# Optimization experiments

Measured on AMD Instinct MI355X. Metric: run time of the kernel, lower is better.

Reference implementation:

```python
import jax, jax.numpy as jnp
import numpy as np
import math

B, N_NODES, N_EDGES = 2, 20000, 320000
IN_DIM, MODEL_DIM, NUM_HEADS = 128, 128, 8
HEAD_DIM = MODEL_DIM // NUM_HEADS
EPS = 1e-5


def setup_inputs() -> dict:
    key = jax.random.key(0)
    ks = jax.random.split(key, 12)
    s = 0.02
    x = jax.random.normal(ks[0], (B, N_NODES, IN_DIM), dtype=jnp.float32)
    edge_index = jax.random.randint(ks[1], (2, N_EDGES), 0, N_NODES, dtype=jnp.int32)
    return {
        "x": x,
        "proj_w": jax.random.normal(ks[2], (IN_DIM, MODEL_DIM), jnp.float32) * s,
        "wq_w": jax.random.normal(ks[3], (MODEL_DIM, MODEL_DIM), jnp.float32) * s,
        "wq_b": jax.random.normal(ks[4], (MODEL_DIM,), jnp.float32) * s,
        "wk_w": jax.random.normal(ks[5], (MODEL_DIM, MODEL_DIM), jnp.float32) * s,
        "wk_b": jax.random.normal(ks[6], (MODEL_DIM,), jnp.float32) * s,
        "wv_w": jax.random.normal(ks[7], (MODEL_DIM, MODEL_DIM), jnp.float32) * s,
        "wv_b": jax.random.normal(ks[8], (MODEL_DIM,), jnp.float32) * s,
        "ln_g": jnp.ones((MODEL_DIM,), jnp.float32),
        "ln_b": jnp.zeros((MODEL_DIM,), jnp.float32),
        "edge_index": edge_index,
    }


def reference(x, proj_w, wq_w, wq_b, wk_w, wk_b, wv_w, wv_b, ln_g, ln_b, edge_index):
    src, dst = edge_index[0], edge_index[1]
    scale = 1.0 / math.sqrt(HEAD_DIM)

    h = x @ proj_w                      # [B, N, D]  (dropout = identity in eval)
    lifted = h[:, src, :]               # [B, E, D] edge gather
    Q = lifted @ wq_w + wq_b
    K = lifted @ wk_w + wk_b
    V = lifted @ wv_w + wv_b

    alpha = jnp.sum(Q * K, axis=-1) * scale  # [B, E]

    def seg_softmax(a):  # a: [E]
        m = jax.ops.segment_max(a, dst, num_segments=N_NODES)
        m = jnp.where(jnp.isfinite(m), m, 0.0)
        e = jnp.exp(a - m[dst])
        s = jax.ops.segment_sum(e, dst, num_segments=N_NODES)
        return e / s[dst]

    attn = jax.vmap(seg_softmax)(alpha)           # [B, E]
    weighted_V = V * attn[..., None]              # [B, E, D]

    seg_sum = lambda t: jax.ops.segment_sum(t, dst, num_segments=N_NODES)
    agg = jax.vmap(seg_sum)(weighted_V)           # [B, N, D]

    counts = jax.ops.segment_sum(jnp.ones((N_EDGES,), jnp.float32), dst,
                                 num_segments=N_NODES)
    skip = jax.vmap(seg_sum)(lifted) / jnp.maximum(counts, 1.0)[None, :, None]

    out = agg + skip
    mu = jnp.mean(out, axis=-1, keepdims=True)
    var = jnp.var(out, axis=-1, keepdims=True)
    return (out - mu) * jax.lax.rsqrt(var + EPS) * ln_g + ln_b
```

## Files before the change

### kernel.cpp

```cpp
#include <hip/hip_runtime.h>
#include <hip/hip_bf16.h>

#define NNODES 20000
#define NEDGES 320000
#define BATCH  2
#define D      128
#define EPSF   1e-5f
#define QTILE_M 64
#define XS_LD   136
#define MAXDEG 64

typedef __attribute__((ext_vector_type(8))) short bf16x8;
typedef __attribute__((ext_vector_type(4))) float f32x4;

static __device__ __forceinline__ unsigned short f2bf(float f) {
    __hip_bfloat16 h = __float2bfloat16(f);
    return *reinterpret_cast<unsigned short*>(&h);
}
static __device__ __forceinline__ float bfu(unsigned short u) {
    union { unsigned int i; float f; } cv;
    cv.i = ((unsigned int)u) << 16;
    return cv.f;
}

__global__ __launch_bounds__(256) void prep_kernel(
    const float* __restrict__ Wp, const float* __restrict__ Wq,
    const float* __restrict__ Wk, const float* __restrict__ Wv,
    unsigned short* __restrict__ WF)
{
    int sg = blockIdx.x * 256 + threadIdx.x;
    int mat = sg >> 11, rem = sg & 2047;
    int f = rem >> 6, l = rem & 63;
    int nt = f >> 2, ks = f & 3;
    int c = l & 15, g = l >> 4;
    const float* W = (mat == 0) ? Wp : (mat == 1) ? Wq : (mat == 2) ? Wk : Wv;
    int n = nt * 16 + c;
    #pragma unroll
    for (int i = 0; i < 8; ++i) {
        int k = ks * 32 + g * 8 + i;
        WF[(size_t)sg * 8 + i] = f2bf(W[k * 128 + n]);
    }
}

__global__ __launch_bounds__(256) void scatter_pad_kernel(
    const int* __restrict__ src, const int* __restrict__ dst,
    const float* __restrict__ a,
    int* __restrict__ cursor,
    int* __restrict__ srcs_pad,
    float* __restrict__ aval)
{
    int e = blockIdx.x * 256 + threadIdx.x;
    if (e >= NEDGES) return;
    int d = dst[e], s = src[e];
    int slot = atomicAdd(&cursor[d], 1);
    if (slot < MAXDEG) {
        int p = d * MAXDEG + slot;
        srcs_pad[p] = s;
        aval[p] = a[s];
        aval[NNODES * MAXDEG + p] = a[NNODES + s];
    }
}

__global__ __launch_bounds__(256) void qkv_mfma_kernel(
    const float* __restrict__ x,
    const unsigned short* __restrict__ WF,
    const float* __restrict__ Bq, const float* __restrict__ Bk, const float* __restrict__ Bv,
    unsigned short* __restrict__ h_out,
    unsigned short* __restrict__ hv_out,
    float* __restrict__ a_out)
{
    __shared__ unsigned short Wbuf[16384];
    __shared__ unsigned short Hs[QTILE_M][XS_LD];
    const int t = threadIdx.x;
    const long row0 = (long)blockIdx.x * QTILE_M;
    const int w = t >> 6, l = t & 63;
    const int g = l >> 4, c = l & 15;
    const int rw = w * 16;

    #define STAGE_W(MAT_OFF)                                            \
        _Pragma("unroll")                                               \
        for (int q = 0; q < 8; ++q) {                                   \
            int s = q * 256 + t;                                        \
            *(bf16x8*)&Wbuf[s * 8] = *(const bf16x8*)(WF + (MAT_OFF) + s * 8); \
        }

    bf16x8 ax[4];
    {
        const float* xr = x + (row0 + rw + c) * D;
        #pragma unroll
        for (int ks = 0; ks < 4; ++ks) {
            float4 u0 = *(const float4*)(xr + ks * 32 + g * 8);
            float4 u1 = *(const float4*)(xr + ks * 32 + g * 8 + 4);
            bf16x8 f;
            f[0] = (short)f2bf(u0.x); f[1] = (short)f2bf(u0.y);
            f[2] = (short)f2bf(u0.z); f[3] = (short)f2bf(u0.w);
            f[4] = (short)f2bf(u1.x); f[5] = (short)f2bf(u1.y);
            f[6] = (short)f2bf(u1.z); f[7] = (short)f2bf(u1.w);
            ax[ks] = f;
        }
    }

    STAGE_W(0)
    __syncthreads();

    f32x4 hacc[8];
    #pragma unroll
    for (int nt = 0; nt < 8; ++nt) hacc[nt] = f32x4{0.f, 0.f, 0.f, 0.f};
    #pragma unroll
    for (int nt = 0; nt < 8; ++nt)
        #pragma unroll
        for (int ks = 0; ks < 4; ++ks) {
            bf16x8 b = *(const bf16x8*)&Wbuf[((nt * 4 + ks) * 64 + l) * 8];
            hacc[nt] = __builtin_amdgcn_mfma_f32_16x16x32_bf16(ax[ks], b, hacc[nt], 0, 0, 0);
        }
    #pragma unroll
    for (int nt = 0; nt < 8; ++nt)
        #pragma unroll
        for (int i = 0; i < 4; ++i)
            Hs[rw + 4 * g + i][nt * 16 + c] = f2bf(hacc[nt][i]);
    __syncthreads();

    #pragma unroll
    for (int q = 0; q < 4; ++q) {
        int ch = t + q * 256;
        int r = ch >> 4, off = (ch & 15) << 3;
        *(bf16x8*)(h_out + (row0 + r) * D + off) = *(const bf16x8*)&Hs[r][off];
    }
    bf16x8 ah[4];
    #pragma unroll
    for (int ks = 0; ks < 4; ++ks)
        ah[ks] = *(const bf16x8*)&Hs[rw + c][ks * 32 + g * 8];
    STAGE_W(16384)
    __syncthreads();

    f32x4 qacc[8];
    #pragma unroll
    for (int nt = 0; nt < 8; ++nt) qacc[nt] = f32x4{0.f, 0.f, 0.f, 0.f};
    #pragma unroll
    for (int nt = 0; nt < 8; ++nt)
        #pragma unroll
        for (int ks = 0; ks < 4; ++ks) {
            bf16x8 b = *(const bf16x8*)&Wbuf[((nt * 4 + ks) * 64 + l) * 8];
            qacc[nt] = __builtin_amdgcn_mfma_f32_16x16x32_bf16(ah[ks], b, qacc[nt], 0, 0, 0);
        }
    __syncthreads();
    STAGE_W(32768)
    __syncthreads();

    f32x4 kacc[8];
    #pragma unroll
    for (int nt = 0; nt < 8; ++nt) kacc[nt] = f32x4{0.f, 0.f, 0.f, 0.f};
    #pragma unroll
    for (int nt = 0; nt < 8; ++nt)
        #pragma unroll
        for (int ks = 0; ks < 4; ++ks) {
            bf16x8 b = *(const bf16x8*)&Wbuf[((nt * 4 + ks) * 64 + l) * 8];
            kacc[nt] = __builtin_amdgcn_mfma_f32_16x16x32_bf16(ah[ks], b, kacc[nt], 0, 0, 0);
        }
    __syncthreads();
    STAGE_W(49152)

    {
        float p[4] = {0.f, 0.f, 0.f, 0.f};
        #pragma unroll
        for (int nt = 0; nt < 8; ++nt) {
            float bq = Bq[nt * 16 + c];
            float bk = Bk[nt * 16 + c];
            #pragma unroll
            for (int i = 0; i < 4; ++i)
                p[i] += (qacc[nt][i] + bq) * (kacc[nt][i] + bk);
        }
        #pragma unroll
        for (int off = 1; off < 16; off <<= 1)
            #pragma unroll
            for (int i = 0; i < 4; ++i) p[i] += __shfl_xor(p[i], off, 64);
        if (c == 0)
            #pragma unroll
            for (int i = 0; i < 4; ++i)
                a_out[row0 + rw + 4 * g + i] = p[i] * 0.25f;
    }
    __syncthreads();

    f32x4 vacc[8];
    #pragma unroll
    for (int nt = 0; nt < 8; ++nt) vacc[nt] = f32x4{0.f, 0.f, 0.f, 0.f};
    #pragma unroll
    for (int nt = 0; nt < 8; ++nt)
        #pragma unroll
        for (int ks = 0; ks < 4; ++ks) {
            bf16x8 b = *(const bf16x8*)&Wbuf[((nt * 4 + ks) * 64 + l) * 8];
            vacc[nt] = __builtin_amdgcn_mfma_f32_16x16x32_bf16(ah[ks], b, vacc[nt], 0, 0, 0);
        }
    #pragma unroll
    for (int nt = 0; nt < 8; ++nt) {
        float bv = Bv[nt * 16 + c];
        #pragma unroll
        for (int i = 0; i < 4; ++i)
            Hs[rw + 4 * g + i][nt * 16 + c] = f2bf(vacc[nt][i] + bv);
    }
    __syncthreads();
    #pragma unroll
    for (int q = 0; q < 4; ++q) {
        int ch = t + q * 256;
        int r = ch >> 4, off = (ch & 15) << 3;
        *(bf16x8*)(hv_out + (row0 + r) * D + off) = *(const bf16x8*)&Hs[r][off];
    }
    #undef STAGE_W
}


__global__ __launch_bounds__(256) void agg_kernel(
    const unsigned short* __restrict__ hb,
    const unsigned short* __restrict__ hvb,
    const float* __restrict__ aval,
    const int* __restrict__ deg_arr,
    const int* __restrict__ srcs_pad,
    const float* __restrict__ ln_g, const float* __restrict__ ln_b,
    float* __restrict__ out)
{
    const int t = threadIdx.x;
    const int w = t >> 6, l = t & 63;
    const int flat = blockIdx.x * 4 + w;
    const int n = flat % NNODES;
    const int b = flat / NNODES;
    const int bN = b * NNODES;
    const int deg = min(deg_arr[n], MAXDEG);
    const int base = n * MAXDEG;
    const bool valid = l < deg;

    int   sr_l = valid ? srcs_pad[base + l] : 0;
    float av_l = valid ? aval[b * (NNODES * MAXDEG) + base + l] : -1e30f;

    float m = av_l;
    #pragma unroll
    for (int off = 32; off >= 1; off >>= 1) m = fmaxf(m, __shfl_xor(m, off, 64));
    float e_l = valid ? __expf(av_l - m) : 0.f;
    float s = e_l;
    #pragma unroll
    for (int off = 32; off >= 1; off >>= 1) s += __shfl_xor(s, off, 64);
    const float inv_s = (deg > 0) ? 1.f / s : 0.f;
    const float inv_d = 1.f / (float)max(deg, 1);
    const float w_l = e_l * inv_s;

    const int q4 = l >> 4;
    const int cq = l & 15;
    float acc[8] = {0,0,0,0,0,0,0,0};
    float sk [8] = {0,0,0,0,0,0,0,0};
    const long rowArr = (long)bN * D;

    const int iters = (deg + 3) >> 2;
    for (int jj = 0; jj < iters; ++jj) {
        int sel = (jj << 2) + q4;
        bool ev = sel < deg;
        int selc = ev ? sel : 0;
        int srj  = __shfl(sr_l, selc, 64);
        float wj = __shfl(w_l,  selc, 64);
        wj = ev ? wj : 0.f;
        float skw = ev ? 1.f : 0.f;
        long ofs = rowArr + (long)srj * D + (cq << 3);
        bf16x8 hv8 = *(const bf16x8*)(hvb + ofs);
        bf16x8 h8  = *(const bf16x8*)(hb + ofs);
        #pragma unroll
        for (int i = 0; i < 8; ++i) {
            acc[i] += wj  * bfu((unsigned short)hv8[i]);
            sk[i]  += skw * bfu((unsigned short)h8[i]);
        }
    }

    #pragma unroll
    for (int i = 0; i < 8; ++i) {
        acc[i] += __shfl_xor(acc[i], 32, 64);
        sk[i]  += __shfl_xor(sk[i],  32, 64);
        acc[i] += __shfl_xor(acc[i], 16, 64);
        sk[i]  += __shfl_xor(sk[i],  16, 64);
    }
    float v[8];
    float sum = 0.f, sq = 0.f;
    #pragma unroll
    for (int i = 0; i < 8; ++i) {
        v[i] = acc[i] + sk[i] * inv_d;
        sum += v[i];
        sq  += v[i] * v[i];
    }
    #pragma unroll
    for (int off = 8; off >= 1; off >>= 1) {
        sum += __shfl_xor(sum, off, 64);
        sq  += __shfl_xor(sq,  off, 64);
    }
    float mu   = sum * (1.f / 128.f);
    float var  = sq * (1.f / 128.f) - mu * mu;
    float rstd = rsqrtf(var + EPSF);
    if (q4 == 0) {
        float4 g0 = *(const float4*)(ln_g + (cq << 3));
        float4 g1 = *(const float4*)(ln_g + (cq << 3) + 4);
        float4 b0 = *(const float4*)(ln_b + (cq << 3));
        float4 b1 = *(const float4*)(ln_b + (cq << 3) + 4);
        float4 o0, o1;
        o0.x = (v[0] - mu) * rstd * g0.x + b0.x;
        o0.y = (v[1] - mu) * rstd * g0.y + b0.y;
        o0.z = (v[2] - mu) * rstd * g0.z + b0.z;
        o0.w = (v[3] - mu) * rstd * g0.w + b0.w;
        o1.x = (v[4] - mu) * rstd * g1.x + b1.x;
        o1.y = (v[5] - mu) * rstd * g1.y + b1.y;
        o1.z = (v[6] - mu) * rstd * g1.z + b1.z;
        o1.w = (v[7] - mu) * rstd * g1.w + b1.w;
        float* op = out + (long)flat * D + (cq << 3);
        *(float4*)op = o0;
        *(float4*)(op + 4) = o1;
    }
}


extern "C" void kernel_launch(void* const* d_in, const int* in_sizes, int n_in,
                              void* d_out, int out_size, void* d_ws, size_t ws_size,
                              hipStream_t stream)
{
    const float* x    = (const float*)d_in[0];
    const float* Wp   = (const float*)d_in[1];
    const float* Wq   = (const float*)d_in[2];
    const float* Bq   = (const float*)d_in[3];
    const float* Wk   = (const float*)d_in[4];
    const float* Bk   = (const float*)d_in[5];
    const float* Wv   = (const float*)d_in[6];
    const float* Bv   = (const float*)d_in[7];
    const float* ln_g = (const float*)d_in[8];
    const float* ln_b = (const float*)d_in[9];
    const int*   ei   = (const int*)d_in[10];
    const int* esrc = ei;
    const int* edst = ei + NEDGES;
    float* out = (float*)d_out;

    char* p = (char*)d_ws;
    auto alloc = [&](size_t bytes) -> char* {
        char* r = p;
        p += (bytes + 255) & ~(size_t)255;
        return r;
    };
    unsigned short* hb  = (unsigned short*)alloc((size_t)BATCH * NNODES * D * 2);
    unsigned short* hvb = (unsigned short*)alloc((size_t)BATCH * NNODES * D * 2);
    float* a        = (float*)alloc((size_t)BATCH * NNODES * 4);
    int* cursor     = (int*)alloc((size_t)NNODES * 4);
    int* srcs_pad   = (int*)alloc((size_t)NNODES * MAXDEG * 4);
    float* aval     = (float*)alloc((size_t)BATCH * NNODES * MAXDEG * 4);
    unsigned short* WF = (unsigned short*)alloc((size_t)4 * 128 * 128 * 2);

    hipMemsetAsync(cursor, 0, (size_t)NNODES * 4, stream);
    prep_kernel<<<32, 256, 0, stream>>>(Wp, Wq, Wk, Wv, WF);
    qkv_mfma_kernel<<<(BATCH * NNODES) / QTILE_M, 256, 0, stream>>>(
        x, WF, Bq, Bk, Bv, hb, hvb, a);
    scatter_pad_kernel<<<(NEDGES + 255) / 256, 256, 0, stream>>>(
        esrc, edst, a, cursor, srcs_pad, aval);
    agg_kernel<<<(BATCH * NNODES) / 4, 256, 0, stream>>>(
        hb, hvb, aval, cursor, srcs_pad, ln_g, ln_b, out);
}
```

Baseline: 177.6 us.

## Interleave h/hv rows, drop aval buffer, fuse cursor clear, prefetch weights and gathers

Stores h and hv interleaved in one 256-wide row so each gathered source node reads one contiguous 512-byte span. The scatter kernel no longer writes the per-edge aval array; agg_kernel instead looks up the attention score a[src] itself. The cursor memset is folded into prep_kernel and scatter now runs before the QKV kernel. The next weight matrix is preloaded into registers while the current one is used, and the agg gather loop is software-pipelined by one iteration. Together these cut launches, global traffic and exposed latency, at the cost of more registers and an extra dependent load in agg.

Result: faster. 164.4 us (-7.4%).

```diff
diff --git a/kernel.cpp b/kernel.cpp
--- a/kernel.cpp
+++ b/kernel.cpp
@@ -26,47 +26,47 @@
 __global__ __launch_bounds__(256) void prep_kernel(
     const float* __restrict__ Wp, const float* __restrict__ Wq,
     const float* __restrict__ Wk, const float* __restrict__ Wv,
-    unsigned short* __restrict__ WF)
-{
-    int sg = blockIdx.x * 256 + threadIdx.x;
-    int mat = sg >> 11, rem = sg & 2047;
-    int f = rem >> 6, l = rem & 63;
-    int nt = f >> 2, ks = f & 3;
-    int c = l & 15, g = l >> 4;
-    const float* W = (mat == 0) ? Wp : (mat == 1) ? Wq : (mat == 2) ? Wk : Wv;
-    int n = nt * 16 + c;
-    #pragma unroll
-    for (int i = 0; i < 8; ++i) {
-        int k = ks * 32 + g * 8 + i;
-        WF[(size_t)sg * 8 + i] = f2bf(W[k * 128 + n]);
+    unsigned short* __restrict__ WF,
+    int* __restrict__ cursor)
+{
+    int bid = blockIdx.x;
+    if (bid < 32) {
+        int sg = bid * 256 + threadIdx.x;
+        int mat = sg >> 11, rem = sg & 2047;
+        int f = rem >> 6, l = rem & 63;
+        int nt = f >> 2, ks = f & 3;
+        int c = l & 15, g = l >> 4;
+        const float* W = (mat == 0) ? Wp : (mat == 1) ? Wq : (mat == 2) ? Wk : Wv;
+        int n = nt * 16 + c;
+        #pragma unroll
+        for (int i = 0; i < 8; ++i) {
+            int k = ks * 32 + g * 8 + i;
+            WF[(size_t)sg * 8 + i] = f2bf(W[k * 128 + n]);
+        }
+    } else {
+        int idx = (bid - 32) * 256 + threadIdx.x;
+        if (idx < NNODES) cursor[idx] = 0;
     }
 }
 
 __global__ __launch_bounds__(256) void scatter_pad_kernel(
     const int* __restrict__ src, const int* __restrict__ dst,
-    const float* __restrict__ a,
     int* __restrict__ cursor,
-    int* __restrict__ srcs_pad,
-    float* __restrict__ aval)
+    int* __restrict__ srcs_pad)
 {
     int e = blockIdx.x * 256 + threadIdx.x;
     if (e >= NEDGES) return;
     int d = dst[e], s = src[e];
     int slot = atomicAdd(&cursor[d], 1);
-    if (slot < MAXDEG) {
-        int p = d * MAXDEG + slot;
-        srcs_pad[p] = s;
-        aval[p] = a[s];
-        aval[NNODES * MAXDEG + p] = a[NNODES + s];
-    }
-}
+    if (slot < MAXDEG) srcs_pad[d * MAXDEG + slot] = s;
+}
+
 
 __global__ __launch_bounds__(256) void qkv_mfma_kernel(
     const float* __restrict__ x,
     const unsigned short* __restrict__ WF,
     const float* __restrict__ Bq, const float* __restrict__ Bk, const float* __restrict__ Bv,
-    unsigned short* __restrict__ h_out,
-    unsigned short* __restrict__ hv_out,
+    unsigned short* __restrict__ hhv,
     float* __restrict__ a_out)
 {
     __shared__ unsigned short Wbuf[16384];
@@ -77,12 +77,17 @@
     const int g = l >> 4, c = l & 15;
     const int rw = w * 16;
 
-    #define STAGE_W(MAT_OFF)                                            \
+    bf16x8 wreg[8];
+    #define LOAD_W_REGS(MAT_OFF)                                        \
         _Pragma("unroll")                                               \
-        for (int q = 0; q < 8; ++q) {                                   \
-            int s = q * 256 + t;                                        \
-            *(bf16x8*)&Wbuf[s * 8] = *(const bf16x8*)(WF + (MAT_OFF) + s * 8); \
-        }
+        for (int q = 0; q < 8; ++q)                                     \
+            wreg[q] = *(const bf16x8*)(WF + (MAT_OFF) + (q * 256 + t) * 8);
+    #define WRITE_W_LDS()                                               \
+        _Pragma("unroll")                                               \
+        for (int q = 0; q < 8; ++q)                                     \
+            *(bf16x8*)&Wbuf[(q * 256 + t) * 8] = wreg[q];
+
+    LOAD_W_REGS(0)
 
     bf16x8 ax[4];
     {
@@ -100,8 +105,9 @@
         }
     }
 
-    STAGE_W(0)
-    __syncthreads();
+    WRITE_W_LDS();
+    __syncthreads();
+    LOAD_W_REGS(16384)
 
     f32x4 hacc[8];
     #pragma unroll
@@ -124,14 +130,16 @@
     for (int q = 0; q < 4; ++q) {
         int ch = t + q * 256;
         int r = ch >> 4, off = (ch & 15) << 3;
-        *(bf16x8*)(h_out + (row0 + r) * D + off) = *(const bf16x8*)&Hs[r][off];
+        *(bf16x8*)(hhv + (row0 + r) * 256 + off) = *(const bf16x8*)&Hs[r][off];
     }
     bf16x8 ah[4];
     #pragma unroll
     for (int ks = 0; ks < 4; ++ks)
         ah[ks] = *(const bf16x8*)&Hs[rw + c][ks * 32 + g * 8];
-    STAGE_W(16384)
-    __syncthreads();
+
+    WRITE_W_LDS();
+    __syncthreads();
+    LOAD_W_REGS(32768)
 
     f32x4 qacc[8];
     #pragma unroll
@@ -144,8 +152,10 @@
             qacc[nt] = __builtin_amdgcn_mfma_f32_16x16x32_bf16(ah[ks], b, qacc[nt], 0, 0, 0);
         }
     __syncthreads();
-    STAGE_W(32768)
-    __syncthreads();
+
+    WRITE_W_LDS();
+    __syncthreads();
+    LOAD_W_REGS(49152)
 
     f32x4 kacc[8];
     #pragma unroll
@@ -158,7 +168,9 @@
             kacc[nt] = __builtin_amdgcn_mfma_f32_16x16x32_bf16(ah[ks], b, kacc[nt], 0, 0, 0);
         }
     __syncthreads();
-    STAGE_W(49152)
+
+    WRITE_W_LDS();
+    __syncthreads();
 
     {
         float p[4] = {0.f, 0.f, 0.f, 0.f};
@@ -179,7 +191,6 @@
             for (int i = 0; i < 4; ++i)
                 a_out[row0 + rw + 4 * g + i] = p[i] * 0.25f;
     }
-    __syncthreads();
 
     f32x4 vacc[8];
     #pragma unroll
@@ -203,16 +214,16 @@
     for (int q = 0; q < 4; ++q) {
         int ch = t + q * 256;
         int r = ch >> 4, off = (ch & 15) << 3;
-        *(bf16x8*)(hv_out + (row0 + r) * D + off) = *(const bf16x8*)&Hs[r][off];
-    }
-    #undef STAGE_W
+        *(bf16x8*)(hhv + (row0 + r) * 256 + 128 + off) = *(const bf16x8*)&Hs[r][off];
+    }
+    #undef LOAD_W_REGS
+    #undef WRITE_W_LDS
 }
 
 
 __global__ __launch_bounds__(256) void agg_kernel(
-    const unsigned short* __restrict__ hb,
-    const unsigned short* __restrict__ hvb,
-    const float* __restrict__ aval,
+    const unsigned short* __restrict__ hhv,
+    const float* __restrict__ a,
     const int* __restrict__ deg_arr,
     const int* __restrict__ srcs_pad,
     const float* __restrict__ ln_g, const float* __restrict__ ln_b,
@@ -225,11 +236,10 @@
     const int b = flat / NNODES;
     const int bN = b * NNODES;
     const int deg = min(deg_arr[n], MAXDEG);
-    const int base = n * MAXDEG;
     const bool valid = l < deg;
 
-    int   sr_l = valid ? srcs_pad[base + l] : 0;
-    float av_l = valid ? aval[b * (NNODES * MAXDEG) + base + l] : -1e30f;
+    int   sr_l = valid ? srcs_pad[n * MAXDEG + l] : 0;
+    float av_l = valid ? a[bN + sr_l] : -1e30f;
 
     float m = av_l;
     #pragma unroll
@@ -246,24 +256,48 @@
     const int cq = l & 15;
     float acc[8] = {0,0,0,0,0,0,0,0};
     float sk [8] = {0,0,0,0,0,0,0,0};
-    const long rowArr = (long)bN * D;
-
-    const int iters = (deg + 3) >> 2;
-    for (int jj = 0; jj < iters; ++jj) {
-        int sel = (jj << 2) + q4;
-        bool ev = sel < deg;
-        int selc = ev ? sel : 0;
-        int srj  = __shfl(sr_l, selc, 64);
-        float wj = __shfl(w_l,  selc, 64);
-        wj = ev ? wj : 0.f;
-        float skw = ev ? 1.f : 0.f;
-        long ofs = rowArr + (long)srj * D + (cq << 3);
-        bf16x8 hv8 = *(const bf16x8*)(hvb + ofs);
-        bf16x8 h8  = *(const bf16x8*)(hb + ofs);
+    const long rowArr = (long)bN * 256 + (cq << 3);
+
+    if (deg > 0) {
+        const int iters = (deg + 3) >> 2;
+        long of0; float wj0, sw0;
+        {
+            int sel = q4;
+            bool ev = sel < deg;
+            int selc = ev ? sel : 0;
+            int srj = __shfl(sr_l, selc, 64);
+            float wj = __shfl(w_l, selc, 64);
+            wj0 = ev ? wj : 0.f;
+            sw0 = ev ? 1.f : 0.f;
+            of0 = rowArr + (long)srj * 256;
+        }
+        bf16x8 h0  = *(const bf16x8*)(hhv + of0);
+        bf16x8 hv0 = *(const bf16x8*)(hhv + of0 + 128);
+        for (int jj = 0; jj < iters - 1; ++jj) {
+            long of1; float wj1, sw1;
+            {
+                int sel = ((jj + 1) << 2) + q4;
+                bool ev = sel < deg;
+                int selc = ev ? sel : 0;
+                int srj = __shfl(sr_l, selc, 64);
+                float wj = __shfl(w_l, selc, 64);
+                wj1 = ev ? wj : 0.f;
+                sw1 = ev ? 1.f : 0.f;
+                of1 = rowArr + (long)srj * 256;
+            }
+            bf16x8 h1  = *(const bf16x8*)(hhv + of1);
+            bf16x8 hv1 = *(const bf16x8*)(hhv + of1 + 128);
+            #pragma unroll
+            for (int i = 0; i < 8; ++i) {
+                acc[i] += wj0 * bfu((unsigned short)hv0[i]);
+                sk[i]  += sw0 * bfu((unsigned short)h0[i]);
+            }
+            h0 = h1; hv0 = hv1; wj0 = wj1; sw0 = sw1;
+        }
         #pragma unroll
         for (int i = 0; i < 8; ++i) {
-            acc[i] += wj  * bfu((unsigned short)hv8[i]);
-            sk[i]  += skw * bfu((unsigned short)h8[i]);
+            acc[i] += wj0 * bfu((unsigned short)hv0[i]);
+            sk[i]  += sw0 * bfu((unsigned short)h0[i]);
         }
     }
 
@@ -336,20 +370,16 @@
         p += (bytes + 255) & ~(size_t)255;
         return r;
     };
-    unsigned short* hb  = (unsigned short*)alloc((size_t)BATCH * NNODES * D * 2);
-    unsigned short* hvb = (unsigned short*)alloc((size_t)BATCH * NNODES * D * 2);
+    unsigned short* hhv = (unsigned short*)alloc((size_t)BATCH * NNODES * 256 * 2);
     float* a        = (float*)alloc((size_t)BATCH * NNODES * 4);
     int* cursor     = (int*)alloc((size_t)NNODES * 4);
     int* srcs_pad   = (int*)alloc((size_t)NNODES * MAXDEG * 4);
-    float* aval     = (float*)alloc((size_t)BATCH * NNODES * MAXDEG * 4);
     unsigned short* WF = (unsigned short*)alloc((size_t)4 * 128 * 128 * 2);
 
-    hipMemsetAsync(cursor, 0, (size_t)NNODES * 4, stream);
-    prep_kernel<<<32, 256, 0, stream>>>(Wp, Wq, Wk, Wv, WF);
+    prep_kernel<<<111, 256, 0, stream>>>(Wp, Wq, Wk, Wv, WF, cursor);
+    scatter_pad_kernel<<<(NEDGES + 255) / 256, 256, 0, stream>>>(esrc, edst, cursor, srcs_pad);
     qkv_mfma_kernel<<<(BATCH * NNODES) / QTILE_M, 256, 0, stream>>>(
-        x, WF, Bq, Bk, Bv, hb, hvb, a);
-    scatter_pad_kernel<<<(NEDGES + 255) / 256, 256, 0, stream>>>(
-        esrc, edst, a, cursor, srcs_pad, aval);
+        x, WF, Bq, Bk, Bv, hhv, a);
     agg_kernel<<<(BATCH * NNODES) / 4, 256, 0, stream>>>(
-        hb, hvb, aval, cursor, srcs_pad, ln_g, ln_b, out);
-}
+        hhv, a, cursor, srcs_pad, ln_g, ln_b, out);
+}
```
